# Kernel optimization log

Hardware: AMD Instinct MI355X
Metric: run time of the kernel (lower is better)

## Reference

```python
import jax, jax.numpy as jnp
import numpy as np

# Constants from the module definition / init args
TOP_M = 10      # args.top_m
HEADS = 4       # nn.MultiheadAttention(512, 4)
EMBED = 512
HEAD_DIM = EMBED // HEADS


def setup_inputs() -> dict:
    key = jax.random.key(0)
    ks = jax.random.split(key, 6)
    B, T, N, C = 16, 60, 196, 512
    visual_patch_top_k = jax.random.normal(ks[0], (B, T, N, C), dtype=jnp.float32)
    qst_feat = jax.random.normal(ks[1], (B, C), dtype=jnp.float32)
    s = 0.02
    # q/k slices of nn.MultiheadAttention's packed in_proj (v/out_proj/FFN/LN do not
    # affect the module's returned outputs, which depend only on attention weights)
    Wq = jax.random.normal(ks[2], (C, C), dtype=jnp.float32) * s
    bq = jnp.zeros((C,), dtype=jnp.float32)
    Wk = jax.random.normal(ks[3], (C, C), dtype=jnp.float32) * s
    bk = jnp.zeros((C,), dtype=jnp.float32)
    return {"visual_patch_top_k": visual_patch_top_k, "qst_feat": qst_feat,
            "Wq": Wq, "bq": bq, "Wk": Wk, "bk": bk}


def reference(visual_patch_top_k, qst_feat, Wq, bq, Wk, bk):
    B, T, N, C = visual_patch_top_k.shape
    # --- soft_attention_select_3d: batched over T (original loops frame-by-frame) ---
    # q: [B, H, Dh] single query token per batch element
    q = (qst_feat @ Wq.T + bq).reshape(B, HEADS, HEAD_DIM)
    # k: [B, T, N, H, Dh]
    k = (jnp.einsum('btnc,ec->btne', visual_patch_top_k, Wk) + bk
         ).reshape(B, T, N, HEADS, HEAD_DIM)
    scale = 1.0 / jnp.sqrt(jnp.float32(HEAD_DIM))
    scores = jnp.einsum('bhd,btnhd->bhtn', q, k) * scale  # [B, H, T, N]
    attn = jax.nn.softmax(scores, axis=-1)
    # torch MHA returns head-averaged weights; query length is 1
    patch_weights = attn.mean(axis=1)                      # [B, T, N]

    # --- find_top_m (faithful to the original, including its gather bug) ---
    sort_index = jnp.argsort(patch_weights, axis=-1)       # ascending by weight
    top_m_index = sort_index[..., -TOP_M:]                 # top-m patch ids
    top_m_index_sort = jnp.sort(top_m_index, axis=-1)      # ascending by index
    # Original nested loop iterates only top_m_index_sort[0][0] and overwrites the
    # full [:, :] slab each iteration -> only the LAST (largest) index of batch 0,
    # frame 0 survives, broadcast over all (b, t, m).
    p = top_m_index_sort[0, 0, -1]
    sel = jnp.take(visual_patch_top_k, p, axis=2)          # [B, T, C]
    visual_patch_top_m = jnp.broadcast_to(sel[:, :, None, :], (B, T, TOP_M, C))
    visual_patch_feat = visual_patch_top_m.reshape(B, T * TOP_M, C)
    return (visual_patch_top_m, visual_patch_feat)
```

## Files before the change

### kernel.cpp

```cpp
#include <hip/hip_runtime.h>
#include <math.h>

#define BB 16
#define TT 60
#define NN 196
#define CC 512
#define HH 4
#define DD 128
#define TOPM 10

__global__ void k_q(const float* __restrict__ qst, const float* __restrict__ Wq,
                    const float* __restrict__ bq, float* __restrict__ q) {
    int wave = (blockIdx.x * blockDim.x + threadIdx.x) >> 6;
    int lane = threadIdx.x & 63;
    const float4* row = (const float4*)(Wq + (size_t)wave * CC);
    const float4* qs  = (const float4*)qst;
    float acc = 0.f;
#pragma unroll
    for (int j = 0; j < 2; ++j) {
        int c4 = lane * 2 + j;
        float4 w = row[c4];
        float4 xv = qs[c4];
        acc += w.x * xv.x + w.y * xv.y + w.z * xv.z + w.w * xv.w;
    }
#pragma unroll
    for (int off = 32; off; off >>= 1) acc += __shfl_xor(acc, off);
    if (lane == 0) q[wave] = acc + bq[wave];
}

__global__ void k_qw(const float* __restrict__ q, const float* __restrict__ Wk,
                     float* __restrict__ qW) {
    int h  = blockIdx.x >> 3;
    int c  = ((blockIdx.x & 7) << 6) + (threadIdx.x & 63);
    int dg = threadIdx.x >> 6;
    int hd0 = h * DD + dg * 32;
    float acc = 0.f;
#pragma unroll
    for (int i = 0; i < 32; ++i)
        acc += q[hd0 + i] * Wk[(size_t)(hd0 + i) * CC + c];
    __shared__ float red[4][64];
    red[dg][threadIdx.x & 63] = acc;
    __syncthreads();
    if (dg == 0)
        qW[h * CC + c] = red[0][c & 63] + red[1][c & 63] + red[2][c & 63] + red[3][c & 63];
}

__global__ void k_scores(const float* __restrict__ x, const float* __restrict__ qW,
                         float* __restrict__ sc) {
    int n = blockIdx.x;
    int lane = threadIdx.x;
    const float scale = 0.08838834764831845f;
    const float4* xr = (const float4*)(x + (size_t)n * CC);
    int c4a = lane * 2, c4b = c4a + 1;
    float4 xa = xr[c4a], xb = xr[c4b];
#pragma unroll
    for (int h = 0; h < HH; ++h) {
        const float4* qr = (const float4*)(qW + h * CC);
        float4 wa = qr[c4a], wb = qr[c4b];
        float acc = xa.x * wa.x + xa.y * wa.y + xa.z * wa.z + xa.w * wa.w +
                    xb.x * wb.x + xb.y * wb.y + xb.z * wb.z + xb.w * wb.w;
#pragma unroll
        for (int off = 32; off; off >>= 1) acc += __shfl_xor(acc, off);
        if (lane == 0) sc[h * NN + n] = scale * acc;
    }
}

__global__ void __launch_bounds__(256) k_bcast_sel(
        const float* __restrict__ x, const float* __restrict__ sc,
        float* __restrict__ out) {
    __shared__ int sp;
    int tid = threadIdx.x;

    if (tid < 64) {
        int lane = tid;
        float pw0 = 0.f, pw1 = 0.f, pw2 = 0.f, pw3 = 0.f;
#pragma unroll
        for (int h = 0; h < HH; ++h) {
            float s0 = sc[h * NN + lane];
            float s1 = sc[h * NN + lane + 64];
            float s2 = sc[h * NN + lane + 128];
            float s3 = (lane + 192 < NN) ? sc[h * NN + lane + 192] : -1e30f;
            float m = fmaxf(fmaxf(s0, s1), fmaxf(s2, s3));
#pragma unroll
            for (int off = 32; off; off >>= 1) m = fmaxf(m, __shfl_xor(m, off));
            float e0 = expf(s0 - m), e1 = expf(s1 - m), e2 = expf(s2 - m);
            float e3 = (lane + 192 < NN) ? expf(s3 - m) : 0.f;
            float ss = e0 + e1 + e2 + e3;
#pragma unroll
            for (int off = 32; off; off >>= 1) ss += __shfl_xor(ss, off);
            float inv = 1.f / ss;
            pw0 += e0 * inv; pw1 += e1 * inv; pw2 += e2 * inv; pw3 += e3 * inv;
        }
        float v0 = pw0, v1 = pw1, v2 = pw2;
        float v3 = (lane + 192 < NN) ? pw3 : -2e30f;
        int p = -1;
        for (int r = 0; r < TOPM; ++r) {
            float v = -3e30f; int idx = -1;
            if (v0 >= v) { v = v0; idx = lane; }
            if (v1 >= v) { v = v1; idx = lane + 64; }
            if (v2 >= v) { v = v2; idx = lane + 128; }
            if (v3 >= v) { v = v3; idx = lane + 192; }
#pragma unroll
            for (int off = 32; off; off >>= 1) {
                float vo = __shfl_xor(v, off);
                int   io = __shfl_xor(idx, off);
                if (vo > v || (vo == v && io > idx)) { v = vo; idx = io; }
            }
            if ((idx & 63) == lane) {
                int jj = idx >> 6;
                if (jj == 0) v0 = -2e30f;
                else if (jj == 1) v1 = -2e30f;
                else if (jj == 2) v2 = -2e30f;
                else v3 = -2e30f;
            }
            if (idx > p) p = idx;
        }
        if (lane == 0) sp = p;
    }
    __syncthreads();
    int p = sp;

    int gt = blockIdx.x * 256 + tid;
    int bt = gt >> 7;
    int c4 = gt & 127;
    float4 v = ((const float4*)x)[((size_t)bt * NN + p) * 128 + c4];
    float4* o0 = (float4*)out + ((size_t)bt * TOPM) * 128 + c4;
    float4* o1 = o0 + (size_t)BB * TT * TOPM * 128;
#pragma unroll
    for (int m = 0; m < TOPM; ++m) {
        o0[(size_t)m * 128] = v;
        o1[(size_t)m * 128] = v;
    }
}

extern "C" void kernel_launch(void* const* d_in, const int* in_sizes, int n_in,
                              void* d_out, int out_size, void* d_ws, size_t ws_size,
                              hipStream_t stream) {
    const float* x   = (const float*)d_in[0];
    const float* qst = (const float*)d_in[1];
    const float* Wq  = (const float*)d_in[2];
    const float* bq  = (const float*)d_in[3];
    const float* Wk  = (const float*)d_in[4];

    float* ws  = (float*)d_ws;
    float* q   = ws;
    float* qW  = ws + 512;
    float* sc  = ws + 2560;

    k_q        <<<128, 256, 0, stream>>>(qst, Wq, bq, q);
    k_qw       <<<32,  256, 0, stream>>>(q, Wk, qW);
    k_scores   <<<NN,   64, 0, stream>>>(x, qW, sc);
    k_bcast_sel<<<(BB * TT * 128) / 256, 256, 0, stream>>>(x, sc, (float*)d_out);
}
```

Measured before the change: 31.68 us.

## Fuse front-end kernels into one persistent kernel with grid barriers

Merges the q projection, qW projection, score computation and top-m selection into a single 128-block kernel that uses atomic grid barriers, with the last-arriving block doing the selection. The broadcast-copy kernel now reads the selected index from workspace instead of every block recomputing the softmax and top-k. This cuts launch count and removes redundant per-block selection work, at the cost of an extra memset launch and spin-wait barriers that rely on all 128 blocks being co-resident.

```diff
diff --git a/kernel.cpp b/kernel.cpp
--- a/kernel.cpp
+++ b/kernel.cpp
@@ -8,71 +8,104 @@
 #define HH 4
 #define DD 128
 #define TOPM 10
+#define FRONT_BLOCKS 128
 
-__global__ void k_q(const float* __restrict__ qst, const float* __restrict__ Wq,
-                    const float* __restrict__ bq, float* __restrict__ q) {
-    int wave = (blockIdx.x * blockDim.x + threadIdx.x) >> 6;
-    int lane = threadIdx.x & 63;
-    const float4* row = (const float4*)(Wq + (size_t)wave * CC);
-    const float4* qs  = (const float4*)qst;
-    float acc = 0.f;
-#pragma unroll
-    for (int j = 0; j < 2; ++j) {
-        int c4 = lane * 2 + j;
-        float4 w = row[c4];
-        float4 xv = qs[c4];
-        acc += w.x * xv.x + w.y * xv.y + w.z * xv.z + w.w * xv.w;
+#define WS_Q   64
+#define WS_QW  576
+#define WS_SC  2624
+#define WS_P   3408
+
+__device__ __forceinline__ void grid_barrier(int* cnt, int target) {
+    __threadfence();
+    __syncthreads();
+    if (threadIdx.x == 0) {
+        __hip_atomic_fetch_add(cnt, 1, __ATOMIC_RELEASE, __HIP_MEMORY_SCOPE_AGENT);
+        while (__hip_atomic_load(cnt, __ATOMIC_ACQUIRE, __HIP_MEMORY_SCOPE_AGENT) < target) {}
     }
-#pragma unroll
-    for (int off = 32; off; off >>= 1) acc += __shfl_xor(acc, off);
-    if (lane == 0) q[wave] = acc + bq[wave];
+    __syncthreads();
+    __threadfence();
 }
 
-__global__ void k_qw(const float* __restrict__ q, const float* __restrict__ Wk,
-                     float* __restrict__ qW) {
-    int h  = blockIdx.x >> 3;
-    int c  = ((blockIdx.x & 7) << 6) + (threadIdx.x & 63);
-    int dg = threadIdx.x >> 6;
-    int hd0 = h * DD + dg * 32;
-    float acc = 0.f;
+__global__ void __launch_bounds__(256) k_front(
+        const float* __restrict__ x, const float* __restrict__ qst,
+        const float* __restrict__ Wq, const float* __restrict__ bq,
+        const float* __restrict__ Wk, float* __restrict__ ws) {
+    int* cnt = (int*)ws;
+    float* q  = ws + WS_Q;
+    float* qW = ws + WS_QW;
+    float* sc = ws + WS_SC;
+
+    int b = blockIdx.x, tid = threadIdx.x;
+    int wv = tid >> 6, lane = tid & 63;
+
+    {
+        int e = b * 4 + wv;
+        const float4* row = (const float4*)(Wq + (size_t)e * CC);
+        const float4* qs  = (const float4*)qst;
+        float acc = 0.f;
 #pragma unroll
-    for (int i = 0; i < 32; ++i)
-        acc += q[hd0 + i] * Wk[(size_t)(hd0 + i) * CC + c];
-    __shared__ float red[4][64];
-    red[dg][threadIdx.x & 63] = acc;
-    __syncthreads();
-    if (dg == 0)
-        qW[h * CC + c] = red[0][c & 63] + red[1][c & 63] + red[2][c & 63] + red[3][c & 63];
-}
-
-__global__ void k_scores(const float* __restrict__ x, const float* __restrict__ qW,
-                         float* __restrict__ sc) {
-    int n = blockIdx.x;
-    int lane = threadIdx.x;
-    const float scale = 0.08838834764831845f;
-    const float4* xr = (const float4*)(x + (size_t)n * CC);
-    int c4a = lane * 2, c4b = c4a + 1;
-    float4 xa = xr[c4a], xb = xr[c4b];
-#pragma unroll
-    for (int h = 0; h < HH; ++h) {
-        const float4* qr = (const float4*)(qW + h * CC);
-        float4 wa = qr[c4a], wb = qr[c4b];
-        float acc = xa.x * wa.x + xa.y * wa.y + xa.z * wa.z + xa.w * wa.w +
-                    xb.x * wb.x + xb.y * wb.y + xb.z * wb.z + xb.w * wb.w;
+        for (int j = 0; j < 2; ++j) {
+            int c4 = lane * 2 + j;
+            float4 w = row[c4], xv = qs[c4];
+            acc += w.x * xv.x + w.y * xv.y + w.z * xv.z + w.w * xv.w;
+        }
 #pragma unroll
         for (int off = 32; off; off >>= 1) acc += __shfl_xor(acc, off);
-        if (lane == 0) sc[h * NN + n] = scale * acc;
+        if (lane == 0) q[e] = acc + bq[e];
     }
-}
+    grid_barrier(cnt + 0, FRONT_BLOCKS);
 
-__global__ void __launch_bounds__(256) k_bcast_sel(
-        const float* __restrict__ x, const float* __restrict__ sc,
-        float* __restrict__ out) {
-    __shared__ int sp;
-    int tid = threadIdx.x;
+    {
+        int ci = tid & 15, g = tid >> 4;
+        int h = b >> 5;
+        int c = ((b & 31) << 4) + ci;
+        int d0 = g * 8;
+        float acc = 0.f;
+#pragma unroll
+        for (int dd = 0; dd < 8; ++dd) {
+            int hd = h * DD + d0 + dd;
+            acc += q[hd] * Wk[(size_t)hd * CC + c];
+        }
+        __shared__ float redB[16][17];
+        redB[g][ci] = acc;
+        __syncthreads();
+        if (g == 0) {
+            float s = 0.f;
+#pragma unroll
+            for (int k = 0; k < 16; ++k) s += redB[k][ci];
+            qW[h * CC + c] = s;
+        }
+    }
+    grid_barrier(cnt + 16, FRONT_BLOCKS);
 
-    if (tid < 64) {
-        int lane = tid;
+    {
+        const float scale = 0.08838834764831845f;
+        const float4* qr = (const float4*)(qW + wv * CC);
+        int c4a = lane * 2, c4b = c4a + 1;
+        float4 wa = qr[c4a], wb = qr[c4b];
+        for (int n = b; n < NN; n += FRONT_BLOCKS) {
+            const float4* xr = (const float4*)(x + (size_t)n * CC);
+            float4 xa = xr[c4a], xb = xr[c4b];
+            float acc = xa.x * wa.x + xa.y * wa.y + xa.z * wa.z + xa.w * wa.w +
+                        xb.x * wb.x + xb.y * wb.y + xb.z * wb.z + xb.w * wb.w;
+#pragma unroll
+            for (int off = 32; off; off >>= 1) acc += __shfl_xor(acc, off);
+            if (lane == 0) sc[wv * NN + n] = scale * acc;
+        }
+    }
+
+    __shared__ int lastFlag;
+    __threadfence();
+    __syncthreads();
+    if (tid == 0) {
+        int r = __hip_atomic_fetch_add(cnt + 32, 1, __ATOMIC_ACQ_REL, __HIP_MEMORY_SCOPE_AGENT);
+        lastFlag = (r == FRONT_BLOCKS - 1);
+    }
+    __syncthreads();
+    if (!lastFlag) return;
+    __threadfence();
+
+    if (wv == 0) {
         float pw0 = 0.f, pw1 = 0.f, pw2 = 0.f, pw3 = 0.f;
 #pragma unroll
         for (int h = 0; h < HH; ++h) {
@@ -115,12 +148,15 @@
             }
             if (idx > p) p = idx;
         }
-        if (lane == 0) sp = p;
+        if (lane == 0) *(int*)(ws + WS_P) = p;
     }
-    __syncthreads();
-    int p = sp;
+}
 
-    int gt = blockIdx.x * 256 + tid;
+__global__ void __launch_bounds__(256) k_bcast(
+        const float* __restrict__ x, const float* __restrict__ ws,
+        float* __restrict__ out) {
+    int p = *(const int*)(ws + WS_P);
+    int gt = blockIdx.x * 256 + threadIdx.x;
     int bt = gt >> 7;
     int c4 = gt & 127;
     float4 v = ((const float4*)x)[((size_t)bt * NN + p) * 128 + c4];
@@ -142,13 +178,9 @@
     const float* bq  = (const float*)d_in[3];
     const float* Wk  = (const float*)d_in[4];
 
-    float* ws  = (float*)d_ws;
-    float* q   = ws;
-    float* qW  = ws + 512;
-    float* sc  = ws + 2560;
+    float* ws = (float*)d_ws;
 
-    k_q        <<<128, 256, 0, stream>>>(qst, Wq, bq, q);
-    k_qw       <<<32,  256, 0, stream>>>(q, Wk, qW);
-    k_scores   <<<NN,   64, 0, stream>>>(x, qW, sc);
-    k_bcast_sel<<<(BB * TT * 128) / 256, 256, 0, stream>>>(x, sc, (float*)d_out);
+    hipMemsetAsync(d_ws, 0, 256, stream);
+    k_front<<<FRONT_BLOCKS, 256, 0, stream>>>(x, qst, Wq, bq, Wk, ws);
+    k_bcast<<<(BB * TT * 128) / 256, 256, 0, stream>>>(x, ws, (float*)d_out);
 }
```

Measured after the change: 83.09 us. 162% more time.

## Fuse q projection, q·Wk, and score kernels into one front kernel

Applied to the files above, without the earlier changes.

Replaces the three small launches (q projection, q times Wk, per-patch scores) with a single 16-block kernel where each block handles one head and a quarter of the patches, recomputing the per-head q and qW in shared memory. This removes two kernel launches and the global round-trips for the intermediates. In exchange each of the four patch groups redundantly recomputes the head's q and qW, and only 16 blocks run, so parallelism is low.

```diff
diff --git a/kernel.cpp b/kernel.cpp
--- a/kernel.cpp
+++ b/kernel.cpp
@@ -9,59 +9,77 @@
 #define DD 128
 #define TOPM 10
 
-__global__ void k_q(const float* __restrict__ qst, const float* __restrict__ Wq,
-                    const float* __restrict__ bq, float* __restrict__ q) {
-    int wave = (blockIdx.x * blockDim.x + threadIdx.x) >> 6;
-    int lane = threadIdx.x & 63;
-    const float4* row = (const float4*)(Wq + (size_t)wave * CC);
-    const float4* qs  = (const float4*)qst;
-    float acc = 0.f;
+__device__ __forceinline__ float hsum4(float4 v) { return v.x + v.y + v.z + v.w; }
+
+__global__ void __launch_bounds__(512) k_front(
+        const float* __restrict__ x, const float* __restrict__ qst,
+        const float* __restrict__ Wq, const float* __restrict__ bq,
+        const float* __restrict__ Wk, float* __restrict__ sc) {
+    __shared__ float4 pbuf[4][132];
+    __shared__ float  qh[DD];
+    __shared__ float  qWs[CC];
+
+    int b = blockIdx.x, t = threadIdx.x;
+    int h = b & 3, g = b >> 2;
+
+    {
+        int d = t >> 2, qq = t & 3;
+        const float4* row = (const float4*)(Wq + (size_t)(h * DD + d) * CC);
+        const float4* qs  = (const float4*)qst;
+        float4 a = make_float4(0.f, 0.f, 0.f, 0.f);
+        int e0 = qq * 32;
+#pragma unroll 8
+        for (int i = 0; i < 32; ++i) {
+            float4 w = row[e0 + i], v = qs[e0 + i];
+            a.x += w.x * v.x; a.y += w.y * v.y; a.z += w.z * v.z; a.w += w.w * v.w;
+        }
+        pbuf[qq][d] = a;
+    }
+    __syncthreads();
+    if (t < DD)
+        qh[t] = hsum4(pbuf[0][t]) + hsum4(pbuf[1][t]) + hsum4(pbuf[2][t]) +
+                hsum4(pbuf[3][t]) + bq[h * DD + t];
+    __syncthreads();
+
+    {
+        int c4 = t & 127, dg = t >> 7;
+        const float4* wk = (const float4*)(Wk + (size_t)(h * DD + dg * 32) * CC);
+        float4 a = make_float4(0.f, 0.f, 0.f, 0.f);
+#pragma unroll 8
+        for (int i = 0; i < 32; ++i) {
+            float qv = qh[dg * 32 + i];
+            float4 w = wk[(size_t)i * (CC / 4) + c4];
+            a.x += qv * w.x; a.y += qv * w.y; a.z += qv * w.z; a.w += qv * w.w;
+        }
+        pbuf[dg][c4] = a;
+    }
+    __syncthreads();
+    if (t < 128) {
+        float4 s0 = pbuf[0][t], s1 = pbuf[1][t], s2 = pbuf[2][t], s3 = pbuf[3][t];
+        float4 r;
+        r.x = s0.x + s1.x + s2.x + s3.x;
+        r.y = s0.y + s1.y + s2.y + s3.y;
+        r.z = s0.z + s1.z + s2.z + s3.z;
+        r.w = s0.w + s1.w + s2.w + s3.w;
+        ((float4*)qWs)[t] = r;
+    }
+    __syncthreads();
+
+    {
+        int wv = t >> 6, lane = t & 63;
+        const float scale = 0.08838834764831845f;
+        const float4* qw4 = (const float4*)qWs;
+        float4 wa = qw4[lane * 2], wb = qw4[lane * 2 + 1];
+        for (int i = wv; i < 49; i += 8) {
+            int n = g * 49 + i;
+            const float4* xr = (const float4*)(x + (size_t)n * CC);
+            float4 xa = xr[lane * 2], xb = xr[lane * 2 + 1];
+            float acc = xa.x * wa.x + xa.y * wa.y + xa.z * wa.z + xa.w * wa.w +
+                        xb.x * wb.x + xb.y * wb.y + xb.z * wb.z + xb.w * wb.w;
 #pragma unroll
-    for (int j = 0; j < 2; ++j) {
-        int c4 = lane * 2 + j;
-        float4 w = row[c4];
-        float4 xv = qs[c4];
-        acc += w.x * xv.x + w.y * xv.y + w.z * xv.z + w.w * xv.w;
-    }
-#pragma unroll
-    for (int off = 32; off; off >>= 1) acc += __shfl_xor(acc, off);
-    if (lane == 0) q[wave] = acc + bq[wave];
-}
-
-__global__ void k_qw(const float* __restrict__ q, const float* __restrict__ Wk,
-                     float* __restrict__ qW) {
-    int h  = blockIdx.x >> 3;
-    int c  = ((blockIdx.x & 7) << 6) + (threadIdx.x & 63);
-    int dg = threadIdx.x >> 6;
-    int hd0 = h * DD + dg * 32;
-    float acc = 0.f;
-#pragma unroll
-    for (int i = 0; i < 32; ++i)
-        acc += q[hd0 + i] * Wk[(size_t)(hd0 + i) * CC + c];
-    __shared__ float red[4][64];
-    red[dg][threadIdx.x & 63] = acc;
-    __syncthreads();
-    if (dg == 0)
-        qW[h * CC + c] = red[0][c & 63] + red[1][c & 63] + red[2][c & 63] + red[3][c & 63];
-}
-
-__global__ void k_scores(const float* __restrict__ x, const float* __restrict__ qW,
-                         float* __restrict__ sc) {
-    int n = blockIdx.x;
-    int lane = threadIdx.x;
-    const float scale = 0.08838834764831845f;
-    const float4* xr = (const float4*)(x + (size_t)n * CC);
-    int c4a = lane * 2, c4b = c4a + 1;
-    float4 xa = xr[c4a], xb = xr[c4b];
-#pragma unroll
-    for (int h = 0; h < HH; ++h) {
-        const float4* qr = (const float4*)(qW + h * CC);
-        float4 wa = qr[c4a], wb = qr[c4b];
-        float acc = xa.x * wa.x + xa.y * wa.y + xa.z * wa.z + xa.w * wa.w +
-                    xb.x * wb.x + xb.y * wb.y + xb.z * wb.z + xb.w * wb.w;
-#pragma unroll
-        for (int off = 32; off; off >>= 1) acc += __shfl_xor(acc, off);
-        if (lane == 0) sc[h * NN + n] = scale * acc;
+            for (int off = 32; off; off >>= 1) acc += __shfl_xor(acc, off);
+            if (lane == 0) sc[h * NN + n] = scale * acc;
+        }
     }
 }
 
@@ -142,13 +160,8 @@
     const float* bq  = (const float*)d_in[3];
     const float* Wk  = (const float*)d_in[4];
 
-    float* ws  = (float*)d_ws;
-    float* q   = ws;
-    float* qW  = ws + 512;
-    float* sc  = ws + 2560;
+    float* sc = (float*)d_ws;
 
-    k_q        <<<128, 256, 0, stream>>>(qst, Wq, bq, q);
-    k_qw       <<<32,  256, 0, stream>>>(q, Wk, qW);
-    k_scores   <<<NN,   64, 0, stream>>>(x, qW, sc);
+    k_front    <<<16, 512, 0, stream>>>(x, qst, Wq, bq, Wk, sc);
     k_bcast_sel<<<(BB * TT * 128) / 256, 256, 0, stream>>>(x, sc, (float*)d_out);
 }
```

Result: slower. 43.41 us (+37.0%).
